# Performance work log

Hardware: AMD Instinct MI355X
Metric: run time of the kernel (lower is better)

## Reference

```python
import jax, jax.numpy as jnp
import numpy as np

NUM_HEADS = 16
EPS = 1e-6

def _rmsnorm(h, w):
    h32 = h.astype(jnp.float32)
    var = jnp.mean(h32 * h32, axis=-1, keepdims=True)
    return (w * (h32 * jax.lax.rsqrt(var + EPS))).astype(h.dtype)

def setup_inputs() -> dict:
    key = jax.random.key(0)
    ks = jax.random.split(key, 4)
    B, N, C = 16, 1024, 1024
    x = jax.random.normal(ks[0], (B, N, C), dtype=jnp.float32)
    qkv_w = jax.random.normal(ks[1], (3 * C, C), dtype=jnp.float32) * (C ** -0.5)
    proj_w = jax.random.normal(ks[2], (C, C), dtype=jnp.float32) * (C ** -0.5)
    proj_b = jnp.zeros((C,), dtype=jnp.float32)
    q_norm_w = jnp.ones((C // NUM_HEADS,), dtype=jnp.float32)
    k_norm_w = jnp.ones((C // NUM_HEADS,), dtype=jnp.float32)
    return {"x": x, "qkv_w": qkv_w, "proj_w": proj_w, "proj_b": proj_b,
            "q_norm_w": q_norm_w, "k_norm_w": k_norm_w}

def reference(x, qkv_w, proj_w, proj_b, q_norm_w, k_norm_w):
    B, N, C = x.shape
    H = NUM_HEADS
    Dh = C // H
    scale = Dh ** -0.5  # qk_scale default; temperature = 1.0
    # QKV projection (no bias): [B,N,3,H,Dh]
    qkv = (x @ qkv_w.T).reshape(B, N, 3, H, Dh)
    q, k, v = qkv[:, :, 0], qkv[:, :, 1], qkv[:, :, 2]
    # per-head QK RMSNorm (fp32 internally)
    q = _rmsnorm(q, q_norm_w)
    k = _rmsnorm(k, k_norm_w)
    # explicit softmax attention: [B,H,N,N]
    attn = jnp.einsum('bnhd,bmhd->bhnm', q * scale, k)
    attn = jax.nn.softmax(attn, axis=-1)
    out = jnp.einsum('bhnm,bmhd->bnhd', attn, v).reshape(B, N, C)
    return out @ proj_w.T + proj_b
```

## Files before the change

### kernel.cpp

```cpp
#include <hip/hip_runtime.h>
#include <hip/hip_bf16.h>

typedef __attribute__((ext_vector_type(8))) __bf16 bf16x8;
typedef __attribute__((ext_vector_type(4))) __bf16 bf16x4;
typedef __attribute__((ext_vector_type(4))) float f32x4;

#define AS1(p) ((__attribute__((address_space(1))) void*)(p))
#define AS3(p) ((__attribute__((address_space(3))) void*)(p))

__global__ void f2b_kernel(const float4* __restrict__ in, bf16x4* __restrict__ out, int n4) {
    int idx = blockIdx.x * blockDim.x + threadIdx.x;
    int stride = gridDim.x * blockDim.x;
    for (int i = idx; i < n4; i += stride) {
        float4 v = in[i];
        bf16x4 o;
        o[0] = (__bf16)v.x; o[1] = (__bf16)v.y; o[2] = (__bf16)v.z; o[3] = (__bf16)v.w;
        out[i] = o;
    }
}

template<int MODE>
__global__ __launch_bounds__(512, 2)
void gemm256(const __bf16* __restrict__ A, const __bf16* __restrict__ Bw,
             const float* __restrict__ bias, const float* __restrict__ qw,
             const float* __restrict__ kw, float* __restrict__ Cf,
             __bf16* __restrict__ Cb, __bf16* __restrict__ Vt,
             int M, int K, int nbn, int ldc)
{
    __shared__ __bf16 Asl[4][256 * 32];
    __shared__ __bf16 Bsl[4][256 * 32];
    const int tid = threadIdx.x, l = tid & 63, w = tid >> 6;
    const int fr = l & 15, fk = l >> 4;

    const int cpx = gridDim.x >> 3;
    const int wg = (blockIdx.x & 7) * cpx + (blockIdx.x >> 3);
    const int bm = wg / nbn, bn = wg % nbn;

    const __bf16* Ag = A + (size_t)bm * 256 * K;
    const __bf16* Bg = Bw + (size_t)bn * 256 * K;

    const int arow = tid >> 2;
    const int uch = (tid & 3) ^ (arow & 3);
    const size_t ga = (size_t)arow * K + uch * 8;
    const size_t ga2 = ga + (size_t)128 * K;

    const int axc = (fk ^ (fr & 3)) * 16;
    int aoff[8], boff[4];
    #pragma unroll
    for (int m = 0; m < 8; ++m)
        aoff[m] = ((w >> 2) * 128 + m * 16 + fr) * 64 + axc;
    #pragma unroll
    for (int n = 0; n < 4; ++n)
        boff[n] = ((w & 3) * 64 + n * 16 + fr) * 64 + axc;

    f32x4 acc[8][4] = {};

#define STAGE256(S) do {                                                                    \
    const int sb_ = (S) & 3;                                                                \
    __builtin_amdgcn_global_load_lds(AS1(Ag + (size_t)(S) * 32 + ga),                       \
        AS3((char*)&Asl[sb_][0] + tid * 16), 16, 0, 0);                                     \
    __builtin_amdgcn_global_load_lds(AS1(Ag + (size_t)(S) * 32 + ga2),                      \
        AS3((char*)&Asl[sb_][0] + tid * 16 + 8192), 16, 0, 0);                              \
    __builtin_amdgcn_global_load_lds(AS1(Bg + (size_t)(S) * 32 + ga),                       \
        AS3((char*)&Bsl[sb_][0] + tid * 16), 16, 0, 0);                                     \
    __builtin_amdgcn_global_load_lds(AS1(Bg + (size_t)(S) * 32 + ga2),                      \
        AS3((char*)&Bsl[sb_][0] + tid * 16 + 8192), 16, 0, 0);                              \
} while (0)

#define PHASE256(S, VMSTR, DOSTAGE) do {                                                    \
    asm volatile("s_waitcnt vmcnt(" VMSTR ")" ::: "memory");                                \
    __builtin_amdgcn_s_barrier();                                                           \
    __builtin_amdgcn_sched_barrier(0);                                                      \
    const int pb_ = (S) & 3;                                                                \
    bf16x8 af[8], bfv[4];                                                                   \
    _Pragma("unroll")                                                                       \
    for (int m = 0; m < 8; ++m)                                                             \
        af[m] = *(const bf16x8*)((const char*)&Asl[pb_][0] + aoff[m]);                      \
    _Pragma("unroll")                                                                       \
    for (int n = 0; n < 4; ++n)                                                             \
        bfv[n] = *(const bf16x8*)((const char*)&Bsl[pb_][0] + boff[n]);                     \
    if (DOSTAGE) STAGE256((S) + 3);                                                         \
    __builtin_amdgcn_s_setprio(1);                                                          \
    _Pragma("unroll")                                                                       \
    for (int m = 0; m < 8; ++m)                                                             \
        _Pragma("unroll")                                                                   \
        for (int n = 0; n < 4; ++n)                                                         \
            acc[m][n] = __builtin_amdgcn_mfma_f32_16x16x32_bf16(af[m], bfv[n], acc[m][n], 0, 0, 0); \
    __builtin_amdgcn_s_setprio(0);                                                          \
} while (0)

    const int S = K >> 5;
    STAGE256(0); STAGE256(1); STAGE256(2);
    for (int s = 0; s < S - 2; ++s)
        PHASE256(s, "8", (s + 3 < S));
    PHASE256(S - 2, "4", false);
    PHASE256(S - 1, "0", false);
#undef PHASE256
#undef STAGE256

    const int rb0 = bm * 256 + (w >> 2) * 128 + fk * 4;
    const int cb0 = bn * 256 + (w & 3) * 64;

    if (MODE == 1) {
        #pragma unroll
        for (int m = 0; m < 8; ++m)
            #pragma unroll
            for (int n = 0; n < 4; ++n) {
                const int col = cb0 + n * 16 + fr;
                const float bv = bias[col];
                #pragma unroll
                for (int r = 0; r < 4; ++r)
                    Cf[(size_t)(rb0 + m * 16 + r) * ldc + col] = acc[m][n][r] + bv;
            }
    } else {
        const int sect = bn >> 2;
        if (sect < 2) {
            const float* wp = (sect == 0) ? qw : kw;
            float wn[4];
            #pragma unroll
            for (int n = 0; n < 4; ++n) wn[n] = wp[((w & 3) * 64 + n * 16 + fr) & 63];
            #pragma unroll
            for (int m = 0; m < 8; ++m) {
                float sc[4];
                #pragma unroll
                for (int r = 0; r < 4; ++r) {
                    float ps = 0.f;
                    #pragma unroll
                    for (int n = 0; n < 4; ++n) ps += acc[m][n][r] * acc[m][n][r];
                    ps += __shfl_xor(ps, 1); ps += __shfl_xor(ps, 2);
                    ps += __shfl_xor(ps, 4); ps += __shfl_xor(ps, 8);
                    sc[r] = rsqrtf(ps * (1.0f / 64.0f) + 1e-6f);
                    if (sect == 0) sc[r] *= 0.18033688011112042f;
                }
                #pragma unroll
                for (int n = 0; n < 4; ++n)
                    #pragma unroll
                    for (int r = 0; r < 4; ++r)
                        Cb[(size_t)(rb0 + m * 16 + r) * ldc + cb0 + n * 16 + fr] =
                            (__bf16)(acc[m][n][r] * sc[r] * wn[n]);
            }
        } else {
            #pragma unroll
            for (int m = 0; m < 8; ++m) {
                const int tok = rb0 + m * 16;
                const int b = tok >> 10, ntok = tok & 1023;
                #pragma unroll
                for (int n = 0; n < 4; ++n) {
                    const int vd = (bn - 8) * 256 + (w & 3) * 64 + n * 16 + fr;
                    bf16x4 pk;
                    #pragma unroll
                    for (int r = 0; r < 4; ++r) pk[r] = (__bf16)acc[m][n][r];
                    *(bf16x4*)&Vt[((size_t)((b * 16 + (vd >> 6)) * 64 + (vd & 63))) * 1024 + ntok] = pk;
                }
            }
        }
    }
}

__global__ __launch_bounds__(256, 3)
void attn_kernel(const __bf16* __restrict__ qkv, const __bf16* __restrict__ vt,
                 __bf16* __restrict__ ao)
{
    __shared__ __bf16 Ks[2][64 * 64];
    __shared__ __bf16 Vs[2][64 * 64];
    __shared__ __bf16 Pl[4][16 * 64];
    const int tid = threadIdx.x, l = tid & 63, w = tid >> 6;
    const int fr = l & 15, fk = l >> 4;
    const int sw = (fr & 7) << 4;

    const int bi = blockIdx.x;
    const int L = (bi & 7) * 256 + (bi >> 3);
    const int qb = L & 7, h = (L >> 3) & 15, b = L >> 7;

    const __bf16* Kg = qkv + (size_t)b * 1024 * 2048 + 1024 + h * 64;
    const __bf16* Vg = vt + (size_t)((b * 16 + h) * 64) * 1024;
    const int srow = tid >> 3, scp = tid & 7;

    const int c8 = (scp ^ (srow & 7)) * 8;
    const size_t kO0 = (size_t)srow * 2048 + c8, kO1 = kO0 + 32 * 2048;
    const size_t vO0 = (size_t)srow * 1024 + c8, vO1 = vO0 + 32 * 1024;
    char* ksd = (char*)&Ks[0][0] + tid * 16;
    char* vsd = (char*)&Vs[0][0] + tid * 16;

#define STAGE(KP, VP, BUF) do {                                                           \
    __builtin_amdgcn_global_load_lds(AS1((KP) + kO0), AS3(ksd + (BUF) * 8192), 16, 0, 0); \
    __builtin_amdgcn_global_load_lds(AS1((KP) + kO1), AS3(ksd + (BUF) * 8192 + 4096), 16, 0, 0); \
    __builtin_amdgcn_global_load_lds(AS1((VP) + vO0), AS3(vsd + (BUF) * 8192), 16, 0, 0); \
    __builtin_amdgcn_global_load_lds(AS1((VP) + vO1), AS3(vsd + (BUF) * 8192 + 4096), 16, 0, 0); \
} while (0)

    STAGE(Kg, Vg, 0);

    const int qrow0 = b * 1024 + qb * 128 + w * 32;
    bf16x8 qf[2][2];
    #pragma unroll
    for (int qi = 0; qi < 2; ++qi)
        #pragma unroll
        for (int dc = 0; dc < 2; ++dc)
            qf[qi][dc] = *(const bf16x8*)&qkv[(size_t)(qrow0 + qi * 16 + fr) * 2048
                                              + h * 64 + dc * 32 + fk * 8];

    const int kb0 = fr * 128 + ((fk ^ (fr & 7)) * 16);
    const int kb1 = fr * 128 + (((4 + fk) ^ (fr & 7)) * 16);
    const char* KsB = (const char*)&Ks[0][0];
    const char* VsB = (const char*)&Vs[0][0];

    char* Pw = (char*)&Pl[w][0];
    const int pw0 = (fr * 128 + 0 * 32 + fk * 8) ^ sw;
    const int pw1 = (fr * 128 + 1 * 32 + fk * 8) ^ sw;
    const int pw2 = (fr * 128 + 2 * 32 + fk * 8) ^ sw;
    const int pw3 = (fr * 128 + 3 * 32 + fk * 8) ^ sw;
    const int pr0 = (fr * 128 + 0 * 64 + fk * 16) ^ sw;
    const int pr1 = (fr * 128 + 1 * 64 + fk * 16) ^ sw;

    bf16x8 onesf;
    #pragma unroll
    for (int i = 0; i < 8; ++i) onesf[i] = (__bf16)1.0f;

    f32x4 oacc[2][4] = {};
    f32x4 lacc[2] = {};

    const __bf16* kg = Kg;
    const __bf16* vg = Vg;
    __syncthreads();

    for (int kt = 0; kt < 16; ++kt) {
        const int cur = kt & 1;
        if (kt < 15) { kg += 64 * 2048; vg += 64; STAGE(kg, vg, cur ^ 1); }

        const int cb = cur * 8192;
        bf16x8 kf[4][2], vf[4][2];
        #pragma unroll
        for (int n = 0; n < 4; ++n) {
            kf[n][0] = *(const bf16x8*)(KsB + cb + kb0 + n * 2048);
            kf[n][1] = *(const bf16x8*)(KsB + cb + kb1 + n * 2048);
        }
        #pragma unroll
        for (int nd = 0; nd < 4; ++nd) {
            vf[nd][0] = *(const bf16x8*)(VsB + cb + kb0 + nd * 2048);
            vf[nd][1] = *(const bf16x8*)(VsB + cb + kb1 + nd * 2048);
        }

        #pragma unroll
        for (int qi = 0; qi < 2; ++qi) {
            f32x4 sacc[4] = {};
            #pragma unroll
            for (int n = 0; n < 4; ++n)
                #pragma unroll
                for (int dc = 0; dc < 2; ++dc)
                    sacc[n] = __builtin_amdgcn_mfma_f32_16x16x32_bf16(kf[n][dc], qf[qi][dc],
                                                                      sacc[n], 0, 0, 0);

            #pragma unroll
            for (int n = 0; n < 4; ++n) {
                bf16x4 pk;
                #pragma unroll
                for (int r = 0; r < 4; ++r)
                    pk[r] = (__bf16)__builtin_amdgcn_exp2f(sacc[n][r]);
                const int pwn = (n == 0) ? pw0 : (n == 1) ? pw1 : (n == 2) ? pw2 : pw3;
                *(bf16x4*)(Pw + pwn) = pk;
            }

            bf16x8 pf0 = *(const bf16x8*)(Pw + pr0);
            bf16x8 pf1 = *(const bf16x8*)(Pw + pr1);
            lacc[qi] = __builtin_amdgcn_mfma_f32_16x16x32_bf16(pf0, onesf, lacc[qi], 0, 0, 0);
            lacc[qi] = __builtin_amdgcn_mfma_f32_16x16x32_bf16(pf1, onesf, lacc[qi], 0, 0, 0);
            #pragma unroll
            for (int nd = 0; nd < 4; ++nd) {
                oacc[qi][nd] = __builtin_amdgcn_mfma_f32_16x16x32_bf16(pf0, vf[nd][0],
                                                                       oacc[qi][nd], 0, 0, 0);
                oacc[qi][nd] = __builtin_amdgcn_mfma_f32_16x16x32_bf16(pf1, vf[nd][1],
                                                                       oacc[qi][nd], 0, 0, 0);
            }
        }
        __syncthreads();
    }

    #pragma unroll
    for (int qi = 0; qi < 2; ++qi) {
        float inv[4];
        #pragma unroll
        for (int r = 0; r < 4; ++r)
            inv[r] = __builtin_amdgcn_rcpf(lacc[qi][r]);
        #pragma unroll
        for (int nd = 0; nd < 4; ++nd)
            #pragma unroll
            for (int r = 0; r < 4; ++r)
                ao[(size_t)(qrow0 + qi * 16 + fk * 4 + r) * 1024 + h * 64 + nd * 16 + fr] =
                    (__bf16)(oacc[qi][nd][r] * inv[r]);
    }
#undef STAGE
}

extern "C" void kernel_launch(void* const* d_in, const int* in_sizes, int n_in,
                              void* d_out, int out_size, void* d_ws, size_t ws_size,
                              hipStream_t stream)
{
    const float* x      = (const float*)d_in[0];
    const float* qkv_w  = (const float*)d_in[1];
    const float* proj_w = (const float*)d_in[2];
    const float* proj_b = (const float*)d_in[3];
    const float* qnw    = (const float*)d_in[4];
    const float* knw    = (const float*)d_in[5];

    char* ws = (char*)d_ws;
    __bf16* xb    = (__bf16*)(ws);
    __bf16* wqkv  = (__bf16*)(ws + 33554432);
    __bf16* wproj = (__bf16*)(ws + 39845888);
    __bf16* qkv   = (__bf16*)(ws + 41943040);
    __bf16* vt    = (__bf16*)(ws + 109051904);
    __bf16* ao    = (__bf16*)(ws + 142606336);

    f2b_kernel<<<2048, 256, 0, stream>>>((const float4*)x,      (bf16x4*)xb,    16777216 / 4);
    f2b_kernel<<<2048, 256, 0, stream>>>((const float4*)qkv_w,  (bf16x4*)wqkv,  3145728 / 4);
    f2b_kernel<<<1024, 256, 0, stream>>>((const float4*)proj_w, (bf16x4*)wproj, 1048576 / 4);

    gemm256<0><<<768, 512, 0, stream>>>(xb, wqkv, nullptr, qnw, knw,
                                        nullptr, qkv, vt, 16384, 1024, 12, 2048);
    attn_kernel<<<2048, 256, 0, stream>>>(qkv, vt, ao);
    gemm256<1><<<256, 512, 0, stream>>>(ao, wproj, proj_b, nullptr, nullptr,
                                        (float*)d_out, nullptr, nullptr, 16384, 1024, 4, 1024);
}
```

Measured before the change: 268.7 us.

## Double-buffer GEMM LDS fragments in registers and overlap reads with MFMAs

The 256x256 GEMM main loop now loads the next k-step's A/B fragments from LDS into a second register set while the current k-step's MFMAs run. Each iteration splits its MFMA work into two halves and places the LDS reads between them. Global-to-LDS staging is now issued right after the barrier, and the vmcnt waits are retuned so the stage needed for the next read has landed. The aim is to hide LDS read latency behind matrix-core work, at the cost of more registers for the doubled fragment arrays, which could hurt occupancy at launch_bounds(512,2).

```diff
diff --git a/kernel.cpp b/kernel.cpp
--- a/kernel.cpp
+++ b/kernel.cpp
@@ -45,57 +45,78 @@
     const size_t ga2 = ga + (size_t)128 * K;
 
     const int axc = (fk ^ (fr & 3)) * 16;
-    int aoff[8], boff[4];
-    #pragma unroll
-    for (int m = 0; m < 8; ++m)
-        aoff[m] = ((w >> 2) * 128 + m * 16 + fr) * 64 + axc;
-    #pragma unroll
-    for (int n = 0; n < 4; ++n)
-        boff[n] = ((w & 3) * 64 + n * 16 + fr) * 64 + axc;
+    const char* abase = (const char*)&Asl[0][0] + ((w >> 2) * 128 + fr) * 64 + axc;
+    const char* bbase = (const char*)&Bsl[0][0] + ((w & 3) * 64 + fr) * 64 + axc;
 
     f32x4 acc[8][4] = {};
-
-#define STAGE256(S) do {                                                                    \
-    const int sb_ = (S) & 3;                                                                \
-    __builtin_amdgcn_global_load_lds(AS1(Ag + (size_t)(S) * 32 + ga),                       \
+    bf16x8 afr[2][8], bfr[2][4];
+
+#define STAGE256(S_) do {                                                                   \
+    const int sb_ = (S_) & 3;                                                               \
+    __builtin_amdgcn_global_load_lds(AS1(Ag + (size_t)(S_) * 32 + ga),                      \
         AS3((char*)&Asl[sb_][0] + tid * 16), 16, 0, 0);                                     \
-    __builtin_amdgcn_global_load_lds(AS1(Ag + (size_t)(S) * 32 + ga2),                      \
+    __builtin_amdgcn_global_load_lds(AS1(Ag + (size_t)(S_) * 32 + ga2),                     \
         AS3((char*)&Asl[sb_][0] + tid * 16 + 8192), 16, 0, 0);                              \
-    __builtin_amdgcn_global_load_lds(AS1(Bg + (size_t)(S) * 32 + ga),                       \
+    __builtin_amdgcn_global_load_lds(AS1(Bg + (size_t)(S_) * 32 + ga),                      \
         AS3((char*)&Bsl[sb_][0] + tid * 16), 16, 0, 0);                                     \
-    __builtin_amdgcn_global_load_lds(AS1(Bg + (size_t)(S) * 32 + ga2),                      \
+    __builtin_amdgcn_global_load_lds(AS1(Bg + (size_t)(S_) * 32 + ga2),                     \
         AS3((char*)&Bsl[sb_][0] + tid * 16 + 8192), 16, 0, 0);                              \
 } while (0)
 
-#define PHASE256(S, VMSTR, DOSTAGE) do {                                                    \
+#define ITER256(T, P, VMSTR, DOREAD) do {                                                   \
     asm volatile("s_waitcnt vmcnt(" VMSTR ")" ::: "memory");                                \
     __builtin_amdgcn_s_barrier();                                                           \
     __builtin_amdgcn_sched_barrier(0);                                                      \
-    const int pb_ = (S) & 3;                                                                \
-    bf16x8 af[8], bfv[4];                                                                   \
-    _Pragma("unroll")                                                                       \
-    for (int m = 0; m < 8; ++m)                                                             \
-        af[m] = *(const bf16x8*)((const char*)&Asl[pb_][0] + aoff[m]);                      \
-    _Pragma("unroll")                                                                       \
-    for (int n = 0; n < 4; ++n)                                                             \
-        bfv[n] = *(const bf16x8*)((const char*)&Bsl[pb_][0] + boff[n]);                     \
-    if (DOSTAGE) STAGE256((S) + 3);                                                         \
+    if ((T) + 3 < S) STAGE256((T) + 3);                                                     \
+    const char* an_ = abase + (((T) + 1) & 3) * 16384;                                      \
+    const char* bn_ = bbase + (((T) + 1) & 3) * 16384;                                      \
     __builtin_amdgcn_s_setprio(1);                                                          \
     _Pragma("unroll")                                                                       \
-    for (int m = 0; m < 8; ++m)                                                             \
+    for (int m = 0; m < 4; ++m)                                                             \
         _Pragma("unroll")                                                                   \
         for (int n = 0; n < 4; ++n)                                                         \
-            acc[m][n] = __builtin_amdgcn_mfma_f32_16x16x32_bf16(af[m], bfv[n], acc[m][n], 0, 0, 0); \
+            acc[m][n] = __builtin_amdgcn_mfma_f32_16x16x32_bf16(afr[P][m], bfr[P][n],       \
+                                                                acc[m][n], 0, 0, 0);        \
     __builtin_amdgcn_s_setprio(0);                                                          \
+    if (DOREAD) {                                                                           \
+        _Pragma("unroll")                                                                   \
+        for (int m = 0; m < 4; ++m)                                                         \
+            afr[(P) ^ 1][m] = *(const bf16x8*)(an_ + m * 1024);                             \
+        _Pragma("unroll")                                                                   \
+        for (int n = 0; n < 4; ++n)                                                         \
+            bfr[(P) ^ 1][n] = *(const bf16x8*)(bn_ + n * 1024);                             \
+    }                                                                                       \
+    __builtin_amdgcn_s_setprio(1);                                                          \
+    _Pragma("unroll")                                                                       \
+    for (int m = 4; m < 8; ++m)                                                             \
+        _Pragma("unroll")                                                                   \
+        for (int n = 0; n < 4; ++n)                                                         \
+            acc[m][n] = __builtin_amdgcn_mfma_f32_16x16x32_bf16(afr[P][m], bfr[P][n],       \
+                                                                acc[m][n], 0, 0, 0);        \
+    __builtin_amdgcn_s_setprio(0);                                                          \
+    if (DOREAD) {                                                                           \
+        _Pragma("unroll")                                                                   \
+        for (int m = 4; m < 8; ++m)                                                         \
+            afr[(P) ^ 1][m] = *(const bf16x8*)(an_ + m * 1024);                             \
+    }                                                                                       \
 } while (0)
 
     const int S = K >> 5;
     STAGE256(0); STAGE256(1); STAGE256(2);
-    for (int s = 0; s < S - 2; ++s)
-        PHASE256(s, "8", (s + 3 < S));
-    PHASE256(S - 2, "4", false);
-    PHASE256(S - 1, "0", false);
-#undef PHASE256
+    asm volatile("s_waitcnt vmcnt(8)" ::: "memory");
+    __builtin_amdgcn_s_barrier();
+    #pragma unroll
+    for (int m = 0; m < 8; ++m) afr[0][m] = *(const bf16x8*)(abase + m * 1024);
+    #pragma unroll
+    for (int n = 0; n < 4; ++n) bfr[0][n] = *(const bf16x8*)(bbase + n * 1024);
+
+    for (int t = 0; t < S - 2; t += 2) {
+        ITER256(t, 0, "4", 1);
+        ITER256(t + 1, 1, "4", 1);
+    }
+    ITER256(S - 2, 0, "0", 1);
+    ITER256(S - 1, 1, "0", 0);
+#undef ITER256
 #undef STAGE256
 
     const int rb0 = bm * 256 + (w >> 2) * 128 + fk * 4;
```

New measurement: 271.6 us. About the same (+1.1%).
